# Optimization experiments

Measured on AMD Instinct MI355X. Metric: run time of the kernel, lower is better.

## Reference

```python
import jax, jax.numpy as jnp
import numpy as np

N, K, D = 65536, 16, 64
JITTER = 1e-6


def setup_inputs() -> dict:
    key = jax.random.key(0)
    k1, k2 = jax.random.split(key)
    z = jax.random.normal(k1, (N, D), dtype=jnp.float32)
    # gamma: soft mixture responsibilities (rows sum to 1, strictly positive)
    g = jax.random.uniform(k2, (N, K), dtype=jnp.float32, minval=1e-3, maxval=1.0)
    gamma = g / jnp.sum(g, axis=1, keepdims=True)
    return {"z": z, "gamma": gamma}


def reference(z, gamma):
    # --- call(): GMM sufficient statistics ---
    gamma_sum = jnp.sum(gamma, axis=0)                      # [K]
    phi = jnp.mean(gamma, axis=0)                           # [K]
    mu = jnp.einsum('ik,il->kl', gamma, z) / gamma_sum[:, None]   # [K,D]
    # sqrt(gamma)-weighted centered samples: [N,K,D]
    z_centered_w = jnp.sqrt(gamma)[:, :, None] * (z[:, None, :] - mu[None, :, :])
    sigma = jnp.einsum('ikl,ikm->klm', z_centered_w, z_centered_w) \
            / gamma_sum[:, None, None]                      # [K,D,D]
    L = jnp.linalg.cholesky(sigma + JITTER * jnp.eye(D, dtype=sigma.dtype))  # [K,D,D]

    # --- energy() ---
    z_centered = z[:, None, :] - mu[None, :, :]             # [N,K,D]
    # batched lower-triangular solve: L v = z_centered^T  -> v: [K,D,N]
    v = jax.scipy.linalg.solve_triangular(
        L, jnp.transpose(z_centered, (1, 2, 0)), lower=True)
    log_det_sigma = 2.0 * jnp.sum(jnp.log(jnp.diagonal(L, axis1=1, axis2=2)), axis=1)  # [K]
    d = z.shape[1]
    # NOTE: signs match the original TF code exactly (including its +d*log(2pi)+log_det)
    logits = (jnp.log(phi)[:, None]
              - 0.5 * jnp.sum(jnp.square(v), axis=1)
              + d * jnp.log(2.0 * jnp.float32(np.pi))
              + log_det_sigma[:, None])                     # [K,N]
    energies = -jax.scipy.special.logsumexp(logits, axis=0) # [N]
    return energies
```

## Files before the change

kernel.cpp:

```cpp
#include <hip/hip_runtime.h>
#include <math.h>


#define NR 65536
#define NCOMP 16
#define DDIM 64
#define JITTER 1e-6f
#define LOG2PI 1.83787706640934548356f

typedef float f32x4 __attribute__((ext_vector_type(4)));
typedef short s16x8 __attribute__((ext_vector_type(8)));
typedef unsigned short u16x4 __attribute__((ext_vector_type(4)));

#define OFF_ZBF 0ul
#define OFF_ZT  (8ul << 20)
#define OFF_SG  (16ul << 20)
#define OFF_S2P (18ul << 20)
#define OFF_SIG (26ul << 20)
#define OFF_UBF (27ul << 20)
#define OFF_F32 (28ul << 20)

__device__ __forceinline__ float b2f(unsigned short u) {
  return __uint_as_float(((unsigned)u) << 16);
}
__device__ __forceinline__ unsigned short f2bs(float f) {
  unsigned u = __float_as_uint(f);
  return (unsigned short)((u + 0x7fffu + ((u >> 16) & 1u)) >> 16);
}

__global__ __launch_bounds__(256) void prep_kernel(
    const float* __restrict__ z, const float* __restrict__ gamma,
    unsigned short* __restrict__ zbf, unsigned short* __restrict__ ztbf,
    unsigned short* __restrict__ sgbf, float* __restrict__ gsum,
    float* __restrict__ s1) {
  __shared__ unsigned short zt[256][64];
  __shared__ float gt[256][16];
  __shared__ float red[16][16];
  const int t = threadIdx.x;
  const long base = (long)blockIdx.x * 256;

  const float4* z4 = (const float4*)(z + base * 64);
  for (int i = t; i < 4096; i += 256) {
    float4 v = z4[i];
    u16x4 o;
    o[0] = f2bs(v.x); o[1] = f2bs(v.y); o[2] = f2bs(v.z); o[3] = f2bs(v.w);
    int r = i >> 4, c = (i & 15) * 4;
    zt[r][c] = o[0]; zt[r][c + 1] = o[1]; zt[r][c + 2] = o[2]; zt[r][c + 3] = o[3];
    *(u16x4*)(zbf + base * 64 + (long)i * 4) = o;
  }
  const float4* g4 = (const float4*)(gamma + base * 16);
  for (int i = t; i < 1024; i += 256) {
    float4 v = g4[i];
    int r = i >> 2, c = (i & 3) * 4;
    gt[r][c] = v.x; gt[r][c + 1] = v.y; gt[r][c + 2] = v.z; gt[r][c + 3] = v.w;
  }
  __syncthreads();

  {
    int l = t >> 2, rp = t & 3;
    for (int j8 = 0; j8 < 64; j8 += 8) {
      s16x8 o;
#pragma unroll
      for (int u2 = 0; u2 < 8; ++u2) o[u2] = (short)zt[rp * 64 + j8 + u2][l];
      *(s16x8*)(ztbf + (long)l * NR + base + rp * 64 + j8) = o;
    }
  }
  if (t < 128) {
    int k = t >> 3, rp = t & 7;
    for (int j8 = 0; j8 < 32; j8 += 8) {
      s16x8 o;
#pragma unroll
      for (int u2 = 0; u2 < 8; ++u2)
        o[u2] = (short)f2bs(sqrtf(gt[rp * 32 + j8 + u2][k]));
      *(s16x8*)(sgbf + (long)k * NR + base + rp * 32 + j8) = o;
    }
  }
  {
    int k = t & 15, rp = t >> 4;
    float s = 0.f;
#pragma unroll
    for (int j = 0; j < 16; ++j) s += gt[rp * 16 + j][k];
    red[k][rp] = s;
  }
  __syncthreads();
  if (t < 16) {
    float s = 0.f;
#pragma unroll
    for (int c = 0; c < 16; ++c) s += red[t][c];
    atomicAdd(&gsum[t], s);
  }
  {
    int l = t & 63, kq = t >> 6;
    float a0 = 0.f, a1 = 0.f, a2 = 0.f, a3 = 0.f;
    for (int r = 0; r < 256; ++r) {
      float zv = b2f(zt[r][l]);
      const float4 gv = *(const float4*)&gt[r][kq * 4];
      a0 = fmaf(gv.x, zv, a0); a1 = fmaf(gv.y, zv, a1);
      a2 = fmaf(gv.z, zv, a2); a3 = fmaf(gv.w, zv, a3);
    }
    atomicAdd(&s1[(kq * 4 + 0) * 64 + l], a0);
    atomicAdd(&s1[(kq * 4 + 1) * 64 + l], a1);
    atomicAdd(&s1[(kq * 4 + 2) * 64 + l], a2);
    atomicAdd(&s1[(kq * 4 + 3) * 64 + l], a3);
  }
}

__global__ __launch_bounds__(256) void stats_kernel(
    const unsigned short* __restrict__ ztbf,
    const unsigned short* __restrict__ sgbf, float* __restrict__ s2p) {
  __shared__ float s2w[4][4096];
  const int t = threadIdx.x;
  const int bid = blockIdx.x;
  const int xcd = bid & 7, gi = bid >> 3;
  const int chunk = xcd * 4 + (gi & 3);
  const int comp = gi >> 2;
  const int w = t >> 6, la = t & 15, hi = (t & 63) >> 4;
  const long rbase = (long)chunk * 2048 + w * 512;
  f32x4 acc[4][4];
#pragma unroll
  for (int a = 0; a < 4; ++a)
#pragma unroll
    for (int b2 = 0; b2 < 4; ++b2) acc[a][b2] = (f32x4){0.f, 0.f, 0.f, 0.f};

  for (int ks = 0; ks < 16; ++ks) {
    const long r0 = rbase + ks * 32 + hi * 8;
    s16x8 sa = *(const s16x8*)(sgbf + (long)comp * NR + r0);
    float saf[8];
#pragma unroll
    for (int u2 = 0; u2 < 8; ++u2) saf[u2] = b2f((unsigned short)sa[u2]);
    s16x8 sq[4];
#pragma unroll
    for (int T = 0; T < 4; ++T) {
      s16x8 zv = *(const s16x8*)(ztbf + (long)(T * 16 + la) * NR + r0);
#pragma unroll
      for (int u2 = 0; u2 < 8; ++u2)
        sq[T][u2] = (short)f2bs(b2f((unsigned short)zv[u2]) * saf[u2]);
    }
#pragma unroll
    for (int a = 0; a < 4; ++a)
#pragma unroll
      for (int b2 = 0; b2 < 4; ++b2)
        acc[a][b2] = __builtin_amdgcn_mfma_f32_16x16x32_bf16(sq[a], sq[b2],
                                                             acc[a][b2], 0, 0, 0);
  }
#pragma unroll
  for (int a = 0; a < 4; ++a)
#pragma unroll
    for (int b2 = 0; b2 < 4; ++b2)
#pragma unroll
      for (int rg = 0; rg < 4; ++rg)
        s2w[w][(a * 16 + hi * 4 + rg) * 64 + b2 * 16 + la] = acc[a][b2][rg];
  __syncthreads();
  float* outp = s2p + ((long)chunk * NCOMP + comp) * 4096;
  for (int i = t; i < 4096; i += 256)
    outp[i] = (s2w[0][i] + s2w[1][i]) + (s2w[2][i] + s2w[3][i]);
}

__global__ __launch_bounds__(256) void reduce_kernel(
    const float* __restrict__ s2p, const float* __restrict__ gsum,
    const float* __restrict__ s1, float* __restrict__ sigf) {
  const int tid = blockIdx.x * 256 + threadIdx.x;
  const int k = tid >> 12, i = tid & 4095;
  float s = 0.f;
#pragma unroll 8
  for (int c = 0; c < 32; ++c) s += s2p[((long)c * NCOMP + k) * 4096 + i];
  const float gs = gsum[k];
  const int a = i >> 6, b = i & 63;
  const float mua = s1[k * 64 + a] / gs;
  const float mub = s1[k * 64 + b] / gs;
  float v = s / gs - mua * mub;
  if (a == b) v += JITTER;
  sigf[k * 4096 + i] = v;
}

__global__ __launch_bounds__(64) void cholinv_kernel(
    const float* __restrict__ sigf, const float* __restrict__ gsum,
    const float* __restrict__ s1, unsigned short* __restrict__ ubf,
    float* __restrict__ tvec, float* __restrict__ constk) {
  __shared__ float Ut[64][66];
  __shared__ float mu_s[64];
  const int c = threadIdx.x;
  const int k = blockIdx.x;
  const float gs = gsum[k];
  mu_s[c] = s1[k * 64 + c] / gs;

  float col[64], lr[64], ux[64];
  const float* sk = sigf + k * 4096;
#pragma unroll
  for (int m = 0; m < 64; ++m) col[m] = sk[m * 64 + c];

  float ld = 0.f;
#pragma unroll
  for (int j = 0; j < 64; ++j) {
    float cj = col[j];
    float ax = 0.f;
#pragma unroll
    for (int jp = 0; jp < j; ++jp) {
      const float b = __uint_as_float(
          __builtin_amdgcn_readlane(__float_as_uint(lr[jp]), j));
      cj = fmaf(-b, lr[jp], cj);
      ax = fmaf(-b, ux[jp], ax);
    }
    const float p = __uint_as_float(
        __builtin_amdgcn_readlane(__float_as_uint(cj), j));
    const float dinv = rsqrtf(p);
    ld += __log2f(p);
    lr[j] = cj * dinv;
    ux[j] = (((c == j) ? 1.f : 0.f) + ax) * dinv;
  }

#pragma unroll
  for (int j = 0; j < 64; ++j) {
    const unsigned short ub = f2bs(ux[j]);
    Ut[j][c] = b2f(ub);
    ubf[k * 4096 + j * 64 + c] = ub;
  }
  __syncthreads();
  float s = 0.f;
#pragma unroll
  for (int l = 0; l < 64; ++l) s = fmaf(Ut[c][l], mu_s[l], s);
  tvec[k * 64 + c] = s;
  if (c == 0)
    constk[k] = logf(gs / (float)NR) + 64.f * LOG2PI
                + 0.69314718055994530942f * ld;
}

__global__ __launch_bounds__(256) void energy_kernel(
    const unsigned short* __restrict__ zbf, const unsigned short* __restrict__ ubf,
    const float* __restrict__ tvec, const float* __restrict__ constk,
    float* __restrict__ out) {
  const int t = threadIdx.x;
  const int w = t >> 6, la = t & 15, hi = (t & 63) >> 4;
  const long r0 = (long)blockIdx.x * 128 + w * 32;
  float M[2][4], S[2][4];
#pragma unroll
  for (int rs = 0; rs < 2; ++rs)
#pragma unroll
    for (int rg = 0; rg < 4; ++rg) { M[rs][rg] = -3.0e38f; S[rs][rg] = 0.f; }

  for (int comp = 0; comp < NCOMP; ++comp) {
    float tvv[4];
#pragma unroll
    for (int mt = 0; mt < 4; ++mt) tvv[mt] = tvec[comp * 64 + mt * 16 + la];
    const float cst = constk[comp];
    f32x4 acc[2][4];
#pragma unroll
    for (int rs = 0; rs < 2; ++rs)
#pragma unroll
      for (int mt = 0; mt < 4; ++mt) acc[rs][mt] = (f32x4){0.f, 0.f, 0.f, 0.f};
#pragma unroll
    for (int ks = 0; ks < 2; ++ks) {
      const int l0 = ks * 32 + hi * 8;
      s16x8 za[2], ub[4];
#pragma unroll
      for (int rs = 0; rs < 2; ++rs)
        za[rs] = *(const s16x8*)(zbf + (r0 + rs * 16 + la) * 64 + l0);
#pragma unroll
      for (int mt = 0; mt < 4; ++mt)
        ub[mt] = *(const s16x8*)(ubf + ((long)comp * 64 + mt * 16 + la) * 64 + l0);
#pragma unroll
      for (int rs = 0; rs < 2; ++rs)
#pragma unroll
        for (int mt = 0; mt < 4; ++mt)
          acc[rs][mt] = __builtin_amdgcn_mfma_f32_16x16x32_bf16(za[rs], ub[mt],
                                                                acc[rs][mt], 0, 0, 0);
    }
#pragma unroll
    for (int rs = 0; rs < 2; ++rs)
#pragma unroll
      for (int rg = 0; rg < 4; ++rg) {
        float qv = 0.f;
#pragma unroll
        for (int mt = 0; mt < 4; ++mt) {
          float d0 = acc[rs][mt][rg] - tvv[mt];
          qv = fmaf(d0, d0, qv);
        }
        qv += __shfl_xor(qv, 1);
        qv += __shfl_xor(qv, 2);
        qv += __shfl_xor(qv, 4);
        qv += __shfl_xor(qv, 8);
        float lg = cst - 0.5f * qv;
        float Mn = fmaxf(M[rs][rg], lg);
        S[rs][rg] = S[rs][rg] * __expf(M[rs][rg] - Mn) + __expf(lg - Mn);
        M[rs][rg] = Mn;
      }
  }
  if (la == 0) {
#pragma unroll
    for (int rs = 0; rs < 2; ++rs)
#pragma unroll
      for (int rg = 0; rg < 4; ++rg)
        out[r0 + rs * 16 + hi * 4 + rg] = -(M[rs][rg] + __logf(S[rs][rg]));
  }
}

extern "C" void kernel_launch(void* const* d_in, const int* in_sizes, int n_in,
                              void* d_out, int out_size, void* d_ws, size_t ws_size,
                              hipStream_t stream) {
  const float* z = (const float*)d_in[0];
  const float* gamma = (const float*)d_in[1];
  float* out = (float*)d_out;
  char* ws = (char*)d_ws;
  unsigned short* zbf = (unsigned short*)(ws + OFF_ZBF);
  unsigned short* ztbf = (unsigned short*)(ws + OFF_ZT);
  unsigned short* sgbf = (unsigned short*)(ws + OFF_SG);
  float* s2p = (float*)(ws + OFF_S2P);
  float* sigf = (float*)(ws + OFF_SIG);
  unsigned short* ubf = (unsigned short*)(ws + OFF_UBF);
  float* f32a = (float*)(ws + OFF_F32);
  float* gsum = f32a;
  float* s1 = f32a + 16;
  float* tvec = f32a + 16 + 1024;
  float* ck = f32a + 16 + 2048;

  hipMemsetAsync(gsum, 0, (16 + 1024) * sizeof(float), stream);
  hipLaunchKernelGGL(prep_kernel, dim3(256), dim3(256), 0, stream,
                     z, gamma, zbf, ztbf, sgbf, gsum, s1);
  hipLaunchKernelGGL(stats_kernel, dim3(512), dim3(256), 0, stream,
                     ztbf, sgbf, s2p);
  hipLaunchKernelGGL(reduce_kernel, dim3(256), dim3(256), 0, stream,
                     s2p, gsum, s1, sigf);
  hipLaunchKernelGGL(cholinv_kernel, dim3(16), dim3(64), 0, stream,
                     sigf, gsum, s1, ubf, tvec, ck);
  hipLaunchKernelGGL(energy_kernel, dim3(512), dim3(256), 0, stream,
                     zbf, ubf, tvec, ck, out);
}
```

Measured before the change: 161.2 us.

## Fuse reduce into Cholesky kernel, replace atomics with partials, tune loads

The separate reduce kernel is folded into the Cholesky/inverse kernel, which now sums the per-chunk second-moment partials and builds sigma in shared memory. prep_kernel writes per-block partial sums for gamma and the first moment instead of using atomics, which also removes the memset. The stats kernel scales values with packed bf16 conversion via inline asm, and the energy kernel hoists z loads out of the component loop and reads a transposed tvec as a float4. This removes one launch, a memset and atomic contention. In exchange, only 16 blocks now do the whole s2p reduction (about 8 MB), which may serialize on few CUs.

```diff
diff --git a/kernel.cpp b/kernel.cpp
--- a/kernel.cpp
+++ b/kernel.cpp
@@ -16,7 +16,7 @@
 #define OFF_ZT  (8ul << 20)
 #define OFF_SG  (16ul << 20)
 #define OFF_S2P (18ul << 20)
-#define OFF_SIG (26ul << 20)
+#define OFF_S1P (26ul << 20)
 #define OFF_UBF (27ul << 20)
 #define OFF_F32 (28ul << 20)
 
@@ -31,13 +31,13 @@
 __global__ __launch_bounds__(256) void prep_kernel(
     const float* __restrict__ z, const float* __restrict__ gamma,
     unsigned short* __restrict__ zbf, unsigned short* __restrict__ ztbf,
-    unsigned short* __restrict__ sgbf, float* __restrict__ gsum,
-    float* __restrict__ s1) {
+    unsigned short* __restrict__ sgbf, float* __restrict__ s1p) {
   __shared__ unsigned short zt[256][64];
   __shared__ float gt[256][16];
   __shared__ float red[16][16];
   const int t = threadIdx.x;
-  const long base = (long)blockIdx.x * 256;
+  const int bid = blockIdx.x;
+  const long base = (long)bid * 256;
 
   const float4* z4 = (const float4*)(z + base * 64);
   for (int i = t; i < 4096; i += 256) {
@@ -87,7 +87,7 @@
     float s = 0.f;
 #pragma unroll
     for (int c = 0; c < 16; ++c) s += red[t][c];
-    atomicAdd(&gsum[t], s);
+    s1p[(1024 + t) * 256 + bid] = s;
   }
   {
     int l = t & 63, kq = t >> 6;
@@ -98,10 +98,10 @@
       a0 = fmaf(gv.x, zv, a0); a1 = fmaf(gv.y, zv, a1);
       a2 = fmaf(gv.z, zv, a2); a3 = fmaf(gv.w, zv, a3);
     }
-    atomicAdd(&s1[(kq * 4 + 0) * 64 + l], a0);
-    atomicAdd(&s1[(kq * 4 + 1) * 64 + l], a1);
-    atomicAdd(&s1[(kq * 4 + 2) * 64 + l], a2);
-    atomicAdd(&s1[(kq * 4 + 3) * 64 + l], a3);
+    s1p[((kq * 4 + 0) * 64 + l) * 256 + bid] = a0;
+    s1p[((kq * 4 + 1) * 64 + l) * 256 + bid] = a1;
+    s1p[((kq * 4 + 2) * 64 + l) * 256 + bid] = a2;
+    s1p[((kq * 4 + 3) * 64 + l) * 256 + bid] = a3;
   }
 }
 
@@ -124,17 +124,27 @@
 
   for (int ks = 0; ks < 16; ++ks) {
     const long r0 = rbase + ks * 32 + hi * 8;
-    s16x8 sa = *(const s16x8*)(sgbf + (long)comp * NR + r0);
-    float saf[8];
-#pragma unroll
-    for (int u2 = 0; u2 < 8; ++u2) saf[u2] = b2f((unsigned short)sa[u2]);
+    const uint4 sg4 = *(const uint4*)(sgbf + (long)comp * NR + r0);
+    const unsigned sgu[4] = {sg4.x, sg4.y, sg4.z, sg4.w};
+    float gl[4], gh[4];
+#pragma unroll
+    for (int p = 0; p < 4; ++p) {
+      gl[p] = __uint_as_float(sgu[p] << 16);
+      gh[p] = __uint_as_float(sgu[p] & 0xffff0000u);
+    }
     s16x8 sq[4];
 #pragma unroll
     for (int T = 0; T < 4; ++T) {
-      s16x8 zv = *(const s16x8*)(ztbf + (long)(T * 16 + la) * NR + r0);
-#pragma unroll
-      for (int u2 = 0; u2 < 8; ++u2)
-        sq[T][u2] = (short)f2bs(b2f((unsigned short)zv[u2]) * saf[u2]);
+      const uint4 zv = *(const uint4*)(ztbf + (long)(T * 16 + la) * NR + r0);
+      const unsigned zu[4] = {zv.x, zv.y, zv.z, zv.w};
+      unsigned rr[4];
+#pragma unroll
+      for (int p = 0; p < 4; ++p) {
+        const float pl = __uint_as_float(zu[p] << 16) * gl[p];
+        const float ph = __uint_as_float(zu[p] & 0xffff0000u) * gh[p];
+        asm("v_cvt_pk_bf16_f32 %0, %1, %2" : "=v"(rr[p]) : "v"(pl), "v"(ph));
+      }
+      sq[T] = __builtin_bit_cast(s16x8, make_uint4(rr[0], rr[1], rr[2], rr[3]));
     }
 #pragma unroll
     for (int a = 0; a < 4; ++a)
@@ -156,82 +166,112 @@
     outp[i] = (s2w[0][i] + s2w[1][i]) + (s2w[2][i] + s2w[3][i]);
 }
 
-__global__ __launch_bounds__(256) void reduce_kernel(
-    const float* __restrict__ s2p, const float* __restrict__ gsum,
-    const float* __restrict__ s1, float* __restrict__ sigf) {
-  const int tid = blockIdx.x * 256 + threadIdx.x;
-  const int k = tid >> 12, i = tid & 4095;
-  float s = 0.f;
+__global__ __launch_bounds__(256) void cholinv_kernel(
+    const float* __restrict__ s2p, const float* __restrict__ s1p,
+    unsigned short* __restrict__ ubf, float* __restrict__ tvecT,
+    float* __restrict__ constk) {
+  __shared__ float sig[64][65];
+  __shared__ float Ut[64][66];
+  __shared__ float part[4][64];
+  __shared__ float gred[4];
+  __shared__ float mu_s[64];
+  const int t = threadIdx.x, k = blockIdx.x;
+  const int l = t & 63, q = t >> 6;
+
+  float gp = s1p[(1024 + k) * 256 + t];
+#pragma unroll
+  for (int off = 32; off; off >>= 1) gp += __shfl_xor(gp, off);
+  if (l == 0) gred[q] = gp;
+  {
+    const float4* rowp = (const float4*)(s1p + (k * 64 + l) * 256 + q * 64);
+    float4 s4 = {0.f, 0.f, 0.f, 0.f};
+#pragma unroll
+    for (int b = 0; b < 16; ++b) {
+      const float4 v = rowp[b];
+      s4.x += v.x; s4.y += v.y; s4.z += v.z; s4.w += v.w;
+    }
+    part[q][l] = (s4.x + s4.y) + (s4.z + s4.w);
+  }
+  __syncthreads();
+  const float gs = (gred[0] + gred[1]) + (gred[2] + gred[3]);
+  if (t < 64)
+    mu_s[t] = ((part[0][t] + part[1][t]) + (part[2][t] + part[3][t])) / gs;
+  __syncthreads();
+
+  const float ginv = 1.f / gs;
+  for (int s = t; s < 1024; s += 256) {
+    float4 a4 = {0.f, 0.f, 0.f, 0.f};
 #pragma unroll 8
-  for (int c = 0; c < 32; ++c) s += s2p[((long)c * NCOMP + k) * 4096 + i];
-  const float gs = gsum[k];
-  const int a = i >> 6, b = i & 63;
-  const float mua = s1[k * 64 + a] / gs;
-  const float mub = s1[k * 64 + b] / gs;
-  float v = s / gs - mua * mub;
-  if (a == b) v += JITTER;
-  sigf[k * 4096 + i] = v;
-}
-
-__global__ __launch_bounds__(64) void cholinv_kernel(
-    const float* __restrict__ sigf, const float* __restrict__ gsum,
-    const float* __restrict__ s1, unsigned short* __restrict__ ubf,
-    float* __restrict__ tvec, float* __restrict__ constk) {
-  __shared__ float Ut[64][66];
-  __shared__ float mu_s[64];
-  const int c = threadIdx.x;
-  const int k = blockIdx.x;
-  const float gs = gsum[k];
-  mu_s[c] = s1[k * 64 + c] / gs;
-
-  float col[64], lr[64], ux[64];
-  const float* sk = sigf + k * 4096;
-#pragma unroll
-  for (int m = 0; m < 64; ++m) col[m] = sk[m * 64 + c];
-
-  float ld = 0.f;
-#pragma unroll
-  for (int j = 0; j < 64; ++j) {
-    float cj = col[j];
-    float ax = 0.f;
-#pragma unroll
-    for (int jp = 0; jp < j; ++jp) {
-      const float b = __uint_as_float(
-          __builtin_amdgcn_readlane(__float_as_uint(lr[jp]), j));
-      cj = fmaf(-b, lr[jp], cj);
-      ax = fmaf(-b, ux[jp], ax);
-    }
-    const float p = __uint_as_float(
-        __builtin_amdgcn_readlane(__float_as_uint(cj), j));
-    const float dinv = rsqrtf(p);
-    ld += __log2f(p);
-    lr[j] = cj * dinv;
-    ux[j] = (((c == j) ? 1.f : 0.f) + ax) * dinv;
-  }
-
-#pragma unroll
-  for (int j = 0; j < 64; ++j) {
-    const unsigned short ub = f2bs(ux[j]);
-    Ut[j][c] = b2f(ub);
-    ubf[k * 4096 + j * 64 + c] = ub;
-  }
-  __syncthreads();
-  float s = 0.f;
-#pragma unroll
-  for (int l = 0; l < 64; ++l) s = fmaf(Ut[c][l], mu_s[l], s);
-  tvec[k * 64 + c] = s;
-  if (c == 0)
-    constk[k] = logf(gs / (float)NR) + 64.f * LOG2PI
-                + 0.69314718055994530942f * ld;
+    for (int c = 0; c < 32; ++c) {
+      const float4 v = *(const float4*)(s2p + ((long)c * NCOMP + k) * 4096 + s * 4);
+      a4.x += v.x; a4.y += v.y; a4.z += v.z; a4.w += v.w;
+    }
+    const int a = s >> 4, b0 = (s & 15) * 4;
+    const float ma = mu_s[a];
+    sig[a][b0 + 0] = a4.x * ginv - ma * mu_s[b0 + 0] + ((a == b0 + 0) ? JITTER : 0.f);
+    sig[a][b0 + 1] = a4.y * ginv - ma * mu_s[b0 + 1] + ((a == b0 + 1) ? JITTER : 0.f);
+    sig[a][b0 + 2] = a4.z * ginv - ma * mu_s[b0 + 2] + ((a == b0 + 2) ? JITTER : 0.f);
+    sig[a][b0 + 3] = a4.w * ginv - ma * mu_s[b0 + 3] + ((a == b0 + 3) ? JITTER : 0.f);
+  }
+  __syncthreads();
+
+  if (t < 64) {
+    const int c = t;
+    float col[64], lr[64], ux[64];
+#pragma unroll
+    for (int m = 0; m < 64; ++m) col[m] = sig[m][c];
+
+    float ld = 0.f;
+#pragma unroll
+    for (int j = 0; j < 64; ++j) {
+      float cj = col[j];
+      float ax = 0.f;
+#pragma unroll
+      for (int jp = 0; jp < j; ++jp) {
+        const float b = __uint_as_float(
+            __builtin_amdgcn_readlane(__float_as_uint(lr[jp]), j));
+        cj = fmaf(-b, lr[jp], cj);
+        ax = fmaf(-b, ux[jp], ax);
+      }
+      const float p = __uint_as_float(
+          __builtin_amdgcn_readlane(__float_as_uint(cj), j));
+      const float dinv = rsqrtf(p);
+      ld += __log2f(p);
+      lr[j] = cj * dinv;
+      ux[j] = (((c == j) ? 1.f : 0.f) + ax) * dinv;
+    }
+#pragma unroll
+    for (int j = 0; j < 64; ++j) Ut[j][c] = b2f(f2bs(ux[j]));
+    if (c == 0)
+      constk[k] = logf(gs / (float)NR) + 64.f * LOG2PI
+                  + 0.69314718055994530942f * ld;
+  }
+  __syncthreads();
+  for (int idx = t; idx < 4096; idx += 256)
+    ubf[k * 4096 + idx] = f2bs(Ut[idx >> 6][idx & 63]);
+  if (t < 64) {
+    float s = 0.f;
+#pragma unroll
+    for (int l2 = 0; l2 < 64; ++l2) s = fmaf(Ut[t][l2], mu_s[l2], s);
+    tvecT[k * 64 + (t & 15) * 4 + (t >> 4)] = s;
+  }
 }
 
 __global__ __launch_bounds__(256) void energy_kernel(
     const unsigned short* __restrict__ zbf, const unsigned short* __restrict__ ubf,
-    const float* __restrict__ tvec, const float* __restrict__ constk,
+    const float* __restrict__ tvecT, const float* __restrict__ constk,
     float* __restrict__ out) {
   const int t = threadIdx.x;
   const int w = t >> 6, la = t & 15, hi = (t & 63) >> 4;
   const long r0 = (long)blockIdx.x * 128 + w * 32;
+
+  s16x8 za[2][2];
+#pragma unroll
+  for (int rs = 0; rs < 2; ++rs)
+#pragma unroll
+    for (int ks = 0; ks < 2; ++ks)
+      za[rs][ks] = *(const s16x8*)(zbf + (r0 + rs * 16 + la) * 64 + ks * 32 + hi * 8);
+
   float M[2][4], S[2][4];
 #pragma unroll
   for (int rs = 0; rs < 2; ++rs)
@@ -239,9 +279,8 @@
     for (int rg = 0; rg < 4; ++rg) { M[rs][rg] = -3.0e38f; S[rs][rg] = 0.f; }
 
   for (int comp = 0; comp < NCOMP; ++comp) {
-    float tvv[4];
-#pragma unroll
-    for (int mt = 0; mt < 4; ++mt) tvv[mt] = tvec[comp * 64 + mt * 16 + la];
+    const float4 tv4 = ((const float4*)tvecT)[comp * 16 + la];
+    const float tvv[4] = {tv4.x, tv4.y, tv4.z, tv4.w};
     const float cst = constk[comp];
     f32x4 acc[2][4];
 #pragma unroll
@@ -251,10 +290,7 @@
 #pragma unroll
     for (int ks = 0; ks < 2; ++ks) {
       const int l0 = ks * 32 + hi * 8;
-      s16x8 za[2], ub[4];
-#pragma unroll
-      for (int rs = 0; rs < 2; ++rs)
-        za[rs] = *(const s16x8*)(zbf + (r0 + rs * 16 + la) * 64 + l0);
+      s16x8 ub[4];
 #pragma unroll
       for (int mt = 0; mt < 4; ++mt)
         ub[mt] = *(const s16x8*)(ubf + ((long)comp * 64 + mt * 16 + la) * 64 + l0);
@@ -262,7 +298,7 @@
       for (int rs = 0; rs < 2; ++rs)
 #pragma unroll
         for (int mt = 0; mt < 4; ++mt)
-          acc[rs][mt] = __builtin_amdgcn_mfma_f32_16x16x32_bf16(za[rs], ub[mt],
+          acc[rs][mt] = __builtin_amdgcn_mfma_f32_16x16x32_bf16(za[rs][ks], ub[mt],
                                                                 acc[rs][mt], 0, 0, 0);
     }
 #pragma unroll
@@ -305,23 +341,18 @@
   unsigned short* ztbf = (unsigned short*)(ws + OFF_ZT);
   unsigned short* sgbf = (unsigned short*)(ws + OFF_SG);
   float* s2p = (float*)(ws + OFF_S2P);
-  float* sigf = (float*)(ws + OFF_SIG);
+  float* s1p = (float*)(ws + OFF_S1P);
   unsigned short* ubf = (unsigned short*)(ws + OFF_UBF);
   float* f32a = (float*)(ws + OFF_F32);
-  float* gsum = f32a;
-  float* s1 = f32a + 16;
-  float* tvec = f32a + 16 + 1024;
-  float* ck = f32a + 16 + 2048;
-
-  hipMemsetAsync(gsum, 0, (16 + 1024) * sizeof(float), stream);
+  float* tvecT = f32a;
+  float* ck = f32a + 1024;
+
   hipLaunchKernelGGL(prep_kernel, dim3(256), dim3(256), 0, stream,
-                     z, gamma, zbf, ztbf, sgbf, gsum, s1);
+                     z, gamma, zbf, ztbf, sgbf, s1p);
   hipLaunchKernelGGL(stats_kernel, dim3(512), dim3(256), 0, stream,
                      ztbf, sgbf, s2p);
-  hipLaunchKernelGGL(reduce_kernel, dim3(256), dim3(256), 0, stream,
-                     s2p, gsum, s1, sigf);
-  hipLaunchKernelGGL(cholinv_kernel, dim3(16), dim3(64), 0, stream,
-                     sigf, gsum, s1, ubf, tvec, ck);
+  hipLaunchKernelGGL(cholinv_kernel, dim3(16), dim3(256), 0, stream,
+                     s2p, s1p, ubf, tvecT, ck);
   hipLaunchKernelGGL(energy_kernel, dim3(512), dim3(256), 0, stream,
-                     zbf, ubf, tvec, ck, out);
-}
+                     zbf, ubf, tvecT, ck, out);
+}
```

Result: slower. 166.5 us (+3.3%).
